# Optimization experiments

Measured on AMD Instinct MI355X. Metric: run time of the kernel, lower is better.

Reference implementation:

```python
import jax, jax.numpy as jnp
import numpy as np

B, S, D = 4, 2048, 1024
H, A = 16, 64


def setup_inputs() -> dict:
    key = jax.random.key(0)
    ks = jax.random.split(key, 9)
    return {
        "q": jax.random.normal(ks[0], (B, S, D), dtype=jnp.float32),
        "k": jax.random.normal(ks[1], (B, S, D), dtype=jnp.float32),
        "v": jax.random.normal(ks[2], (B, S, D), dtype=jnp.float32),
        "Wq": jax.random.normal(ks[3], (H, D, A), dtype=jnp.float32) * (1.0 / np.sqrt(D)),
        "bq": jax.random.normal(ks[4], (H, A), dtype=jnp.float32) * 0.01,
        "Wk": jax.random.normal(ks[5], (H, D, A), dtype=jnp.float32) * (1.0 / np.sqrt(D)),
        "bk": jax.random.normal(ks[6], (H, A), dtype=jnp.float32) * 0.01,
        "Wv": jax.random.normal(ks[7], (H, D, A), dtype=jnp.float32) * (1.0 / np.sqrt(D)),
        "bv": jax.random.normal(ks[8], (H, A), dtype=jnp.float32) * 0.01,
    }


def reference(q, k, v, Wq, bq, Wk, bk, Wv, bv):
    # Per-head linear projections (batched over heads): [B,H,S,A]
    qh = jnp.einsum("bsd,hda->bhsa", q, Wq) + bq[None, :, None, :]
    kh = jnp.einsum("bsd,hda->bhsa", k, Wk) + bk[None, :, None, :]
    vh = jnp.einsum("bsd,hda->bhsa", v, Wv) + bv[None, :, None, :]
    # NOTE: original has NO 1/sqrt(d) scaling and no mask.
    scores = jnp.einsum("bhqa,bhka->bhqk", qh, kh)  # [B,H,S,S]
    weights = jax.nn.softmax(scores, axis=-1)
    attn = jnp.einsum("bhqk,bhka->bhqa", weights, vh)  # [B,H,S,A]
    # concat heads on last dim: [B,S,H*A]
    return jnp.transpose(attn, (0, 2, 1, 3)).reshape(q.shape[0], q.shape[1], -1)
```

## Files before the change

### kernel.cpp

```cpp
#include <hip/hip_runtime.h>
#include <stdint.h>

#define B_ 4
#define S_ 2048
#define D_ 1024
#define H_ 16
#define A_ 64
#define M_ (B_*S_)
#define BH_ (B_*H_)
#define INV_LN2 1.4426950408889634f

typedef _Float16 f16x8 __attribute__((ext_vector_type(8)));
typedef float    f32x4 __attribute__((ext_vector_type(4)));

__device__ __forceinline__ uint32_t f2h(float f) {
    _Float16 h = (_Float16)f;
    return (uint32_t)__builtin_bit_cast(uint16_t, h);
}

__device__ __forceinline__ float exp2f_fast(float x) {
    return __builtin_amdgcn_exp2f(x);
}

__device__ __forceinline__ uint32_t pkrtz(float a, float b) {
    return __builtin_bit_cast(uint32_t, __builtin_amdgcn_cvt_pkrtz(a, b));
}

__device__ __forceinline__ int swz(int row, int col) {
    return (row * 64 + col) ^ ((row & 7) << 3);
}

__global__ __launch_bounds__(256) void prep_w(
    const float* __restrict__ Wq, const float* __restrict__ Wk, const float* __restrict__ Wv,
    uint16_t* __restrict__ Wt)
{
    __shared__ float tile[64][65];
    const int dt = blockIdx.x, h = blockIdx.y, p = blockIdx.z;
    const float* W = (p == 0) ? Wq : (p == 1) ? Wk : Wv;
    const float sc = (p == 0) ? INV_LN2 : 1.0f;
    const float* src = W + (h * D_ + dt * 64) * A_;
    const int t = threadIdx.x;
    const int r0 = t >> 4, c4 = (t & 15) * 4;
    #pragma unroll
    for (int i = 0; i < 4; i++) {
        int r = r0 + i * 16;
        float4 x = *(const float4*)(src + r * A_ + c4);
        tile[r][c4] = x.x; tile[r][c4 + 1] = x.y; tile[r][c4 + 2] = x.z; tile[r][c4 + 3] = x.w;
    }
    __syncthreads();
    uint16_t* dst = Wt + (p * H_ + h) * (A_ * D_) + dt * 64;
    #pragma unroll
    for (int i = 0; i < 4; i++) {
        int a = r0 + i * 16;
        int d4 = (t & 15) * 4;
        uint2 o2;
        o2.x = f2h(tile[d4][a] * sc)     | (f2h(tile[d4 + 1][a] * sc) << 16);
        o2.y = f2h(tile[d4 + 2][a] * sc) | (f2h(tile[d4 + 3][a] * sc) << 16);
        *(uint2*)(dst + a * D_ + d4) = o2;
    }
}

__global__ __launch_bounds__(512) void proj_kernel(
    const float* __restrict__ qsrc, const float* __restrict__ ksrc, const float* __restrict__ vsrc,
    const uint16_t* __restrict__ Wt,
    const float* __restrict__ bq, const float* __restrict__ bk, const float* __restrict__ bv,
    uint16_t* __restrict__ qh, uint16_t* __restrict__ kh, uint16_t* __restrict__ vpv)
{
    __shared__ __align__(16) uint16_t As[2][128 * 32];
    __shared__ __align__(16) uint16_t Bs[2][256 * 32];
    const int p = blockIdx.z, nt = blockIdx.y, mt = blockIdx.x;
    const int t = threadIdx.x, lane = t & 63, w = t >> 6;
    const int wr = w >> 2, wc = w & 3;
    const int lr = lane & 15, lg = lane >> 4;
    const int Mbase = mt * 128;
    const float* Af = (p == 0) ? qsrc : (p == 1) ? ksrc : vsrc;

    const int ar  = t >> 2;
    const int als = t & 3;
    const int afx = (ar >> 1) & 3;
    const float* asrc = Af + (size_t)(Mbase + ar) * D_ + als * 8;
    const int awoff = ar * 32 + ((als ^ afx) * 8);

    const int bslot = (t & 3) ^ (((t >> 2) >> 1) & 3);
    const uint16_t* bsrc[2];
    #pragma unroll
    for (int i = 0; i < 2; i++) {
        int row = (t >> 2) + 128 * i;
        bsrc[i] = Wt + ((size_t)(p * H_ + nt * 4 + (row >> 6)) * A_ + (row & 63)) * D_ + bslot * 8;
    }

    f32x4 acc[4][4] = {};

    #define BSTAGE(buf, kkv) do {                                                                  \
        __builtin_amdgcn_global_load_lds(bsrc[0] + (kkv), (char*)(&Bs[buf][0]) + w * 1024,        16, 0, 0); \
        __builtin_amdgcn_global_load_lds(bsrc[1] + (kkv), (char*)(&Bs[buf][0]) + 8192 + w * 1024, 16, 0, 0); \
    } while (0)

    #define AWRITE(buf, v0, v1) do {                                                               \
        uint4 u_;                                                                                  \
        u_.x = pkrtz((v0).x, (v0).y); u_.y = pkrtz((v0).z, (v0).w);                                \
        u_.z = pkrtz((v1).x, (v1).y); u_.w = pkrtz((v1).z, (v1).w);                                \
        *(uint4*)(&As[buf][awoff]) = u_;                                                           \
    } while (0)

    {
        BSTAGE(0, 0);
        float4 a0 = *(const float4*)(asrc);
        float4 a1 = *(const float4*)(asrc + 4);
        asm volatile("s_waitcnt vmcnt(0)" ::: "memory");
        AWRITE(0, a0, a1);
        __syncthreads();
    }

    const int NKS = D_ / 32;
    for (int ks = 0; ks < NKS; ks++) {
        const int cur = ks & 1, nxt = cur ^ 1;
        const bool hasNext = (ks + 1 < NKS);
        float4 a0, a1;
        if (hasNext) {
            BSTAGE(nxt, (ks + 1) * 32);
            a0 = *(const float4*)(asrc + (ks + 1) * 32);
            a1 = *(const float4*)(asrc + (ks + 1) * 32 + 4);
        }

        f16x8 af[4], bf[4];
        #pragma unroll
        for (int mb = 0; mb < 4; mb++) {
            const int r = wr * 64 + mb * 16 + lr;
            af[mb] = *(const f16x8*)(&As[cur][r * 32 + ((lg ^ ((r >> 1) & 3)) * 8)]);
        }
        #pragma unroll
        for (int nb = 0; nb < 4; nb++) {
            const int r = wc * 64 + nb * 16 + lr;
            bf[nb] = *(const f16x8*)(&Bs[cur][r * 32 + ((lg ^ ((r >> 1) & 3)) * 8)]);
        }
        #pragma unroll
        for (int mb = 0; mb < 4; mb++) {
            #pragma unroll
            for (int nb = 0; nb < 4; nb++)
                acc[mb][nb] = __builtin_amdgcn_mfma_f32_16x16x32_f16(af[mb], bf[nb], acc[mb][nb], 0, 0, 0);
        }

        if (hasNext) {
            asm volatile("s_waitcnt vmcnt(0)" ::: "memory");
            __builtin_amdgcn_sched_barrier(0);
            AWRITE(nxt, a0, a1);
            __syncthreads();
        }
    }
    #undef BSTAGE
    #undef AWRITE

    const int h = nt * 4 + wc;
    const int b = Mbase >> 11;
    const int bh = b * H_ + h;
    const int sbase = Mbase & (S_ - 1);
    const float* bias = ((p == 0) ? bq : (p == 1) ? bk : bv) + h * A_;
    const float bsc = (p == 0) ? INV_LN2 : 1.0f;
    #pragma unroll
    for (int mb = 0; mb < 4; mb++) {
        #pragma unroll
        for (int nb = 0; nb < 4; nb++) {
            const int a = nb * 16 + lr;
            const float bia = bias[a] * bsc;
            const int s0 = sbase + wr * 64 + mb * 16 + 4 * lg;
            if (p < 2) {
                uint16_t* o = (p == 0) ? qh : kh;
                #pragma unroll
                for (int r = 0; r < 4; r++)
                    o[(bh * S_ + s0 + r) * A_ + a] = (uint16_t)f2h(acc[mb][nb][r] + bia);
            } else {
                const int kt2 = s0 >> 6, kv0 = s0 & 63;
                const int kb2 = kv0 >> 5, jhi = (kv0 >> 4) & 1, lg2 = (kv0 >> 2) & 3;
                uint2 pk2;
                pk2.x = f2h(acc[mb][nb][0] + bia) | (f2h(acc[mb][nb][1] + bia) << 16);
                pk2.y = f2h(acc[mb][nb][2] + bia) | (f2h(acc[mb][nb][3] + bia) << 16);
                *(uint2*)(vpv + ((size_t)((bh * 32 + kt2) * 512 + kb2 * 256 + lg2 * 64 + a)) * 8 + 4 * jhi) = pk2;
            }
        }
    }
}

__global__ __launch_bounds__(512, 8) void flash_kernel(
    const uint16_t* __restrict__ qh, const uint16_t* __restrict__ kh,
    const uint16_t* __restrict__ vpv, float* __restrict__ out)
{
    __shared__ __align__(16) uint16_t smem[24576];
    const int t = threadIdx.x, lane = t & 63, w = t >> 6;
    const int lr = lane & 15, lg = lane >> 4;

    const int flat = blockIdx.y * gridDim.x + blockIdx.x;
    const int nf = (flat & 7) * 128 + (flat >> 3);
    const int qt = nf & 15, bh = nf >> 4;
    const int b = bh >> 4, h = bh & (H_ - 1);

    f16x8 qf[2];
    {
        const uint16_t* qp = qh + (size_t)(bh * S_ + qt * 128 + w * 16 + lr) * A_ + 8 * lg;
        qf[0] = *(const f16x8*)(qp);
        qf[1] = *(const f16x8*)(qp + 32);
    }
    f16x8 ones;
    #pragma unroll
    for (int j = 0; j < 8; j++) ones[j] = (_Float16)1.0f;

    const int row0 = t >> 3;
    const int col0 = (t * 8) & 63;
    const int scol = col0 ^ ((row0 & 7) << 3);
    const uint16_t* kg = kh + (size_t)(bh * S_ + row0) * A_ + scol;
    const uint16_t* vg = vpv + (size_t)bh * (S_ * A_) + t * 8;

    f32x4 negm = {};
    f32x4 oacc[4] = {};
    f32x4 lsum = {};

    #define FSTAGE(buf, kt_) do {                                                         \
        __builtin_amdgcn_global_load_lds(kg + (size_t)(kt_) * (64 * A_),                  \
                                         smem + (buf) * 4096 + w * 512, 16, 0, 0);        \
        __builtin_amdgcn_global_load_lds(vg + (size_t)(kt_) * 4096,                       \
                                         smem + 12288 + (buf) * 4096 + w * 512, 16, 0, 0);\
    } while (0)

    const int NT = S_ / 64;
    FSTAGE(0, 0);
    FSTAGE(1, 1);

    int cur = 0;
    for (int kt = 0; kt < NT; kt++) {
        if (kt < NT - 1) asm volatile("s_waitcnt vmcnt(2)" ::: "memory");
        else             asm volatile("s_waitcnt vmcnt(0)" ::: "memory");
        __builtin_amdgcn_s_barrier();
        __builtin_amdgcn_sched_barrier(0);
        if (kt + 2 < NT) {
            int nb2 = cur + 2; if (nb2 >= 3) nb2 -= 3;
            FSTAGE(nb2, kt + 2);
        }
        __builtin_amdgcn_sched_barrier(0);
        const uint16_t* Kc = smem + cur * 4096;
        const uint16_t* Vc = smem + 12288 + cur * 4096;

        f32x4 sacc[4];
        __builtin_amdgcn_s_setprio(1);
        #pragma unroll
        for (int nb = 0; nb < 4; nb++) {
            f16x8 kf = *(const f16x8*)(Kc + swz(nb * 16 + lr, 8 * lg));
            sacc[nb] = __builtin_amdgcn_mfma_f32_16x16x32_f16(kf, qf[0], negm, 0, 0, 0);
        }
        #pragma unroll
        for (int nb = 0; nb < 4; nb++) {
            f16x8 kf = *(const f16x8*)(Kc + swz(nb * 16 + lr, 32 + 8 * lg));
            sacc[nb] = __builtin_amdgcn_mfma_f32_16x16x32_f16(kf, qf[1], sacc[nb], 0, 0, 0);
        }
        __builtin_amdgcn_s_setprio(0);

        float a0 = fmaxf(fmaxf(sacc[0][0], sacc[0][1]), sacc[0][2]);
        float a1 = fmaxf(fmaxf(sacc[0][3], sacc[1][0]), sacc[1][1]);
        float a2 = fmaxf(fmaxf(sacc[1][2], sacc[1][3]), sacc[2][0]);
        float a3 = fmaxf(fmaxf(sacc[2][1], sacc[2][2]), sacc[2][3]);
        float a4 = fmaxf(fmaxf(sacc[3][0], sacc[3][1]), sacc[3][2]);
        float pm = fmaxf(fmaxf(fmaxf(a0, a1), fmaxf(a2, a3)), fmaxf(a4, sacc[3][3]));

        if (__any(pm > 11.0f)) {
            float tm = fmaxf(pm, __shfl_xor(pm, 16));
            tm = fmaxf(tm, __shfl_xor(tm, 32));
            float delta = fmaxf(tm, 0.0f);
            float sc = exp2f_fast(-delta);
            #pragma unroll
            for (int r = 0; r < 4; r++) negm[r] -= delta;
            #pragma unroll
            for (int nb = 0; nb < 4; nb++) {
                #pragma unroll
                for (int r = 0; r < 4; r++) sacc[nb][r] -= delta;
            }
            float scr[4];
            #pragma unroll
            for (int r = 0; r < 4; r++) scr[r] = __shfl(sc, 4 * lg + r);
            #pragma unroll
            for (int r = 0; r < 4; r++) lsum[r] *= scr[r];
            #pragma unroll
            for (int nb = 0; nb < 4; nb++) {
                #pragma unroll
                for (int r = 0; r < 4; r++) oacc[nb][r] *= scr[r];
            }
        }

        f16x8 paf[2];
        #pragma unroll
        for (int kb2 = 0; kb2 < 2; kb2++) {
            float e[8];
            #pragma unroll
            for (int jh = 0; jh < 2; jh++) {
                #pragma unroll
                for (int r = 0; r < 4; r++)
                    e[jh * 4 + r] = exp2f_fast(sacc[2 * kb2 + jh][r]);
            }
            uint4 u;
            u.x = pkrtz(e[0], e[1]); u.y = pkrtz(e[2], e[3]);
            u.z = pkrtz(e[4], e[5]); u.w = pkrtz(e[6], e[7]);
            paf[kb2] = __builtin_bit_cast(f16x8, u);
        }

        __builtin_amdgcn_s_setprio(1);
        lsum = __builtin_amdgcn_mfma_f32_16x16x32_f16(paf[0], ones, lsum, 0, 0, 0);
        lsum = __builtin_amdgcn_mfma_f32_16x16x32_f16(paf[1], ones, lsum, 0, 0, 0);
        #pragma unroll
        for (int kb2 = 0; kb2 < 2; kb2++) {
            #pragma unroll
            for (int nb = 0; nb < 4; nb++) {
                f16x8 vf = *(const f16x8*)(Vc + ((kb2 * 4 + lg) * 64 + nb * 16 + lr) * 8);
                oacc[nb] = __builtin_amdgcn_mfma_f32_16x16x32_f16(paf[kb2], vf, oacc[nb], 0, 0, 0);
            }
        }
        __builtin_amdgcn_s_setprio(0);

        cur = (cur == 2) ? 0 : cur + 1;
    }
    #undef FSTAGE

    __syncthreads();
    float* outs = (float*)smem;
    #pragma unroll
    for (int r = 0; r < 4; r++) {
        const float inv = 1.0f / lsum[r];
        const int sl = w * 16 + 4 * lg + r;
        #pragma unroll
        for (int nb = 0; nb < 4; nb++)
            outs[sl * 64 + nb * 16 + lr] = oacc[nb][r] * inv;
    }
    __syncthreads();
    const int orow = t >> 4, oslot = t & 15;
    float* obase = out + (size_t)(b * S_ + qt * 128 + orow) * (H_ * A_) + h * A_ + oslot * 4;
    #pragma unroll
    for (int i = 0; i < 4; i++)
        *(float4*)(obase + (size_t)(32 * i) * (H_ * A_)) =
            *(const float4*)(outs + (orow + 32 * i) * 64 + oslot * 4);
}

extern "C" void kernel_launch(void* const* d_in, const int* in_sizes, int n_in,
                              void* d_out, int out_size, void* d_ws, size_t ws_size,
                              hipStream_t stream)
{
    const float* q  = (const float*)d_in[0];
    const float* k  = (const float*)d_in[1];
    const float* v  = (const float*)d_in[2];
    const float* Wq = (const float*)d_in[3];
    const float* bq = (const float*)d_in[4];
    const float* Wk = (const float*)d_in[5];
    const float* bk = (const float*)d_in[6];
    const float* Wv = (const float*)d_in[7];
    const float* bv = (const float*)d_in[8];
    float* out = (float*)d_out;

    uint8_t* ws = (uint8_t*)d_ws;
    const size_t SZ_H  = (size_t)BH_ * S_ * A_ * 2;
    uint16_t* qh  = (uint16_t*)(ws);
    uint16_t* kh  = (uint16_t*)(ws + SZ_H);
    uint16_t* vpv = (uint16_t*)(ws + 2 * SZ_H);
    uint16_t* Wt  = (uint16_t*)(ws + 3 * SZ_H);

    prep_w<<<dim3(16, H_, 3), 256, 0, stream>>>(Wq, Wk, Wv, Wt);
    proj_kernel<<<dim3(M_ / 128, 4, 3), 512, 0, stream>>>(q, k, v, Wt,
                                                          bq, bk, bv, qh, kh, vpv);
    flash_kernel<<<dim3(S_ / 128, BH_), 512, 0, stream>>>(qh, kh, vpv, out);
}
```

Baseline: 171.3 us.

## Deepen A-prefetch in projection GEMM with unrolled double-buffer and partial vmcnt waits

Unrolls the projection GEMM K-loop by two with fixed LDS buffers. The fp32 activation loads for A are now issued two K-steps ahead instead of one, and the code waits with vmcnt(2) instead of draining all outstanding global loads. The aim is to hide global load latency behind MFMA work, since the old loop stalled on vmcnt(0) every step. The price is more live registers for the extra prefetch and hand-counted waitcnts, which must stay matched to the load order.

```diff
diff --git a/kernel.cpp b/kernel.cpp
--- a/kernel.cpp
+++ b/kernel.cpp
@@ -82,18 +82,14 @@
     const int awoff = ar * 32 + ((als ^ afx) * 8);
 
     const int bslot = (t & 3) ^ (((t >> 2) >> 1) & 3);
-    const uint16_t* bsrc[2];
-    #pragma unroll
-    for (int i = 0; i < 2; i++) {
-        int row = (t >> 2) + 128 * i;
-        bsrc[i] = Wt + ((size_t)(p * H_ + nt * 4 + (row >> 6)) * A_ + (row & 63)) * D_ + bslot * 8;
-    }
+    const uint16_t* bsrc0 = Wt + ((size_t)(p * H_ + nt * 4 + ((t >> 2) >> 6)) * A_ + ((t >> 2) & 63)) * D_ + bslot * 8;
+    const uint16_t* bsrc1 = Wt + ((size_t)(p * H_ + nt * 4 + (((t >> 2) + 128) >> 6)) * A_ + ((t >> 2) & 63)) * D_ + bslot * 8;
 
     f32x4 acc[4][4] = {};
 
     #define BSTAGE(buf, kkv) do {                                                                  \
-        __builtin_amdgcn_global_load_lds(bsrc[0] + (kkv), (char*)(&Bs[buf][0]) + w * 1024,        16, 0, 0); \
-        __builtin_amdgcn_global_load_lds(bsrc[1] + (kkv), (char*)(&Bs[buf][0]) + 8192 + w * 1024, 16, 0, 0); \
+        __builtin_amdgcn_global_load_lds(bsrc0 + (kkv), (char*)(&Bs[buf][0]) + w * 1024,        16, 0, 0); \
+        __builtin_amdgcn_global_load_lds(bsrc1 + (kkv), (char*)(&Bs[buf][0]) + 8192 + w * 1024, 16, 0, 0); \
     } while (0)
 
     #define AWRITE(buf, v0, v1) do {                                                               \
@@ -103,53 +99,79 @@
         *(uint4*)(&As[buf][awoff]) = u_;                                                           \
     } while (0)
 
-    {
-        BSTAGE(0, 0);
-        float4 a0 = *(const float4*)(asrc);
-        float4 a1 = *(const float4*)(asrc + 4);
-        asm volatile("s_waitcnt vmcnt(0)" ::: "memory");
-        AWRITE(0, a0, a1);
-        __syncthreads();
-    }
+    #define COMPUTE(buf) do {                                                                      \
+        f16x8 af[4], bf[4];                                                                        \
+        _Pragma("unroll")                                                                          \
+        for (int mb = 0; mb < 4; mb++) {                                                           \
+            const int r = wr * 64 + mb * 16 + lr;                                                  \
+            af[mb] = *(const f16x8*)(&As[buf][r * 32 + ((lg ^ ((r >> 1) & 3)) * 8)]);              \
+        }                                                                                          \
+        _Pragma("unroll")                                                                          \
+        for (int nb = 0; nb < 4; nb++) {                                                           \
+            const int r = wc * 64 + nb * 16 + lr;                                                  \
+            bf[nb] = *(const f16x8*)(&Bs[buf][r * 32 + ((lg ^ ((r >> 1) & 3)) * 8)]);              \
+        }                                                                                          \
+        _Pragma("unroll")                                                                          \
+        for (int mb = 0; mb < 4; mb++) {                                                           \
+            _Pragma("unroll")                                                                      \
+            for (int nb = 0; nb < 4; nb++)                                                         \
+                acc[mb][nb] = __builtin_amdgcn_mfma_f32_16x16x32_f16(af[mb], bf[nb], acc[mb][nb], 0, 0, 0); \
+        }                                                                                          \
+    } while (0)
+
+    float4 e0, e1, o0, o1;
+    BSTAGE(0, 0);
+    __builtin_amdgcn_sched_barrier(0);
+    e0 = *(const float4*)(asrc);
+    e1 = *(const float4*)(asrc + 4);
+    asm volatile("s_waitcnt vmcnt(0)" ::: "memory");
+    AWRITE(0, e0, e1);
+    __syncthreads();
+    o0 = *(const float4*)(asrc + 32);
+    o1 = *(const float4*)(asrc + 36);
+    __builtin_amdgcn_sched_barrier(0);
 
     const int NKS = D_ / 32;
-    for (int ks = 0; ks < NKS; ks++) {
-        const int cur = ks & 1, nxt = cur ^ 1;
-        const bool hasNext = (ks + 1 < NKS);
-        float4 a0, a1;
-        if (hasNext) {
-            BSTAGE(nxt, (ks + 1) * 32);
-            a0 = *(const float4*)(asrc + (ks + 1) * 32);
-            a1 = *(const float4*)(asrc + (ks + 1) * 32 + 4);
-        }
-
-        f16x8 af[4], bf[4];
-        #pragma unroll
-        for (int mb = 0; mb < 4; mb++) {
-            const int r = wr * 64 + mb * 16 + lr;
-            af[mb] = *(const f16x8*)(&As[cur][r * 32 + ((lg ^ ((r >> 1) & 3)) * 8)]);
-        }
-        #pragma unroll
-        for (int nb = 0; nb < 4; nb++) {
-            const int r = wc * 64 + nb * 16 + lr;
-            bf[nb] = *(const f16x8*)(&Bs[cur][r * 32 + ((lg ^ ((r >> 1) & 3)) * 8)]);
-        }
-        #pragma unroll
-        for (int mb = 0; mb < 4; mb++) {
-            #pragma unroll
-            for (int nb = 0; nb < 4; nb++)
-                acc[mb][nb] = __builtin_amdgcn_mfma_f32_16x16x32_f16(af[mb], bf[nb], acc[mb][nb], 0, 0, 0);
-        }
-
-        if (hasNext) {
-            asm volatile("s_waitcnt vmcnt(0)" ::: "memory");
+    for (int ks = 0; ks < NKS; ks += 2) {
+        BSTAGE(1, (ks + 1) * 32);
+        __builtin_amdgcn_sched_barrier(0);
+        if (ks + 2 < NKS) {
+            e0 = *(const float4*)(asrc + (ks + 2) * 32);
+            e1 = *(const float4*)(asrc + (ks + 2) * 32 + 4);
+        }
+        __builtin_amdgcn_sched_barrier(0);
+        COMPUTE(0);
+        if (ks + 2 < NKS) asm volatile("s_waitcnt vmcnt(2)" ::: "memory");
+        else              asm volatile("s_waitcnt vmcnt(0)" ::: "memory");
+        __builtin_amdgcn_sched_barrier(0);
+        AWRITE(1, o0, o1);
+        asm volatile("s_waitcnt lgkmcnt(0)" ::: "memory");
+        __builtin_amdgcn_s_barrier();
+        __builtin_amdgcn_sched_barrier(0);
+
+        if (ks + 2 < NKS) {
+            BSTAGE(0, (ks + 2) * 32);
             __builtin_amdgcn_sched_barrier(0);
-            AWRITE(nxt, a0, a1);
-            __syncthreads();
+            if (ks + 3 < NKS) {
+                o0 = *(const float4*)(asrc + (ks + 3) * 32);
+                o1 = *(const float4*)(asrc + (ks + 3) * 32 + 4);
+            }
+            __builtin_amdgcn_sched_barrier(0);
+        }
+        COMPUTE(1);
+        if (ks + 2 < NKS) {
+            if (ks + 3 < NKS) asm volatile("s_waitcnt vmcnt(2)" ::: "memory");
+            else              asm volatile("s_waitcnt vmcnt(0)" ::: "memory");
+            __builtin_amdgcn_sched_barrier(0);
+            AWRITE(0, e0, e1);
+            asm volatile("s_waitcnt lgkmcnt(0)" ::: "memory");
+            __builtin_amdgcn_s_barrier();
+            __builtin_amdgcn_sched_barrier(0);
         }
     }
     #undef BSTAGE
     #undef AWRITE
+    #undef COMPUTE
 
     const int h = nt * 4 + wc;
     const int b = Mbase >> 11;
```

After: 166.2 us. 1.03x faster.
